# Kernel tuning notes

Measured on AMD Instinct MI355X. Metric: run time of the kernel, lower is better.

Reference implementation:

```python
import jax, jax.numpy as jnp
import numpy as np

N, L = 5, 2097152
WIDTH = 11  # max_pool1d kernel width in the original


def setup_inputs() -> dict:
    key = jax.random.key(0)
    k1, k2 = jax.random.split(key)
    rppg = jax.random.normal(k1, (N, L), dtype=jnp.float32)
    ppg = jax.random.normal(k2, (N, L), dtype=jnp.float32)
    return {"rppg": rppg, "ppg": ppg, "fs": 30, "epoch": 15}


def _normalize(x):
    # normalize_torch: per-signal standardization
    mu = x.mean(axis=1, keepdims=True)
    sd = x.std(axis=1, keepdims=True)
    return (x - mu) / sd


def _window_max(x, width):
    # sliding max over centered window of `width`, same padding (-inf pad)
    return jax.lax.reduce_window(x, -jnp.inf, jax.lax.max,
                                 (1, width), (1, 1),
                                 [(0, 0), (width // 2, width // 2)])


def _mean_hr(x, fs):
    # A position p is a 'nice peak' iff max_pool argmax at p equals p,
    # i.e. x[p] is the max of its own centered window (ties have measure 0
    # for continuous signals). unique()+masking collapses to this mask.
    w = _window_max(x, WIDTH)
    m1 = x == w                                            # [N, L] peak mask
    npk = m1.sum(axis=1, keepdims=True).astype(x.dtype)
    mean_pk = (x * m1).sum(axis=1, keepdims=True) / npk    # mean of peak values
    m = m1 & (x > mean_pk / 2)                             # amplitude-filtered peaks
    idx = jnp.arange(x.shape[1])
    vals = jnp.where(m, idx, -1)
    # previous peak index strictly before p (fixed-shape replacement for diff
    # over a variable-length peak index list)
    prev = jnp.pad(jax.lax.cummax(vals, axis=1)[:, :-1], ((0, 0), (1, 0)),
                   constant_values=-1)
    valid = m & (prev >= 0)                                # one entry per inter-peak gap
    gaps = (idx[None, :] - prev).astype(x.dtype)
    inv = jnp.where(valid, 1.0 / gaps, 0.0)
    # mean(60 / (gap / fs)) = 60 * fs * mean(1 / gap)
    return (60.0 * fs) * inv.sum(axis=1) / valid.sum(axis=1).astype(x.dtype)


def reference(rppg, ppg, fs, epoch):
    ppg = _normalize(ppg.reshape(N, -1))
    rppg = _normalize(rppg.reshape(N, -1))
    ppg_hr = _mean_hr(ppg, fs)
    rppg_hr = _mean_hr(rppg, fs)
    # hr_score = mean_i |ppg_hr - rppg_hr| / ppg_hr  (peak_score is computed
    # in the original but not returned)
    return jnp.mean(jnp.abs(ppg_hr - rppg_hr) / ppg_hr)
```

## Files before the change

### kernel.cpp

```cpp
#include <hip/hip_runtime.h>
#include <math.h>

namespace {

constexpr int LNUM = 2097152;
constexpr int NROW = 5;
constexpr int TPB = 256;
constexpr int CHUNK = 4096;
constexpr int NCHUNK = LNUM / CHUNK;
constexpr int NSERIES = 2 * NROW;
constexpr int NBLK = NSERIES * NCHUNK;
constexpr int NWAVE = TPB / 64;
constexpr int SEG = CHUNK / NWAVE;
constexpr int ITER = SEG / 64;

struct Agg { int first; int last; int c; double s; };

__device__ inline Agg combine(const Agg& a, const Agg& b) {
  Agg r;
  r.first = (a.first >= 0) ? a.first : b.first;
  r.last  = (b.last >= 0) ? b.last : a.last;
  r.s = a.s + b.s;
  r.c = a.c + b.c;
  if (a.last >= 0 && b.first >= 0) {
    r.s += 1.0 / (double)(b.first - a.last);
    r.c += 1;
  }
  return r;
}

__device__ inline void stage(const float* __restrict__ x, int base, float* sh) {
  if (base >= 8 && base + CHUNK + 8 <= LNUM) {
    const float4* xv = (const float4*)(x + base - 8);
    float4* shv = (float4*)sh;
    for (int i = threadIdx.x; i < CHUNK / 4 + 4; i += TPB) shv[i] = xv[i];
  } else {
    for (int i = threadIdx.x; i < CHUNK + 16; i += TPB) {
      int g = base - 8 + i;
      sh[i] = (g >= 0 && g < LNUM) ? x[g] : -INFINITY;
    }
  }
}

__global__ __launch_bounds__(TPB) void stats_kernel(
    const float* __restrict__ rppg, const float* __restrict__ ppg,
    double* __restrict__ psum, double* __restrict__ ppk,
    int* __restrict__ pnpk) {
  __shared__ float sh[CHUNK + 16];
  __shared__ double wsum[NWAVE], wpk[NWAVE];
  __shared__ int wn[NWAVE];
  const int bid = blockIdx.x;
  const int sig = bid / (NROW * NCHUNK);
  const int rem = bid - sig * (NROW * NCHUNK);
  const int row = rem / NCHUNK;
  const int chunk = rem - row * NCHUNK;
  const float* x = (sig == 0 ? rppg : ppg) + (size_t)row * LNUM;
  const int base = chunk * CHUNK;

  stage(x, base, sh);
  __syncthreads();

  const int lane = threadIdx.x & 63;
  const int wid = threadIdx.x >> 6;
  const int woff = wid * SEG;
  double tsum = 0.0, tpk = 0.0;
  int tn = 0;
  for (int j = 0; j < ITER; ++j) {
    int pl = woff + j * 64 + lane;
    float v = sh[pl + 8];
    float w = sh[pl + 3];
#pragma unroll
    for (int k = 1; k < 11; ++k) w = fmaxf(w, sh[pl + 3 + k]);
    tsum += (double)v;
    if (v == w) { tpk += (double)v; ++tn; }
  }
  for (int off = 32; off > 0; off >>= 1) {
    tsum += __shfl_down(tsum, off);
    tpk  += __shfl_down(tpk, off);
    tn   += __shfl_down(tn, off);
  }
  if (lane == 0) { wsum[wid] = tsum; wpk[wid] = tpk; wn[wid] = tn; }
  __syncthreads();
  if (threadIdx.x == 0) {
    double S = 0.0, P = 0.0; int Nn = 0;
    for (int wq = 0; wq < NWAVE; ++wq) { S += wsum[wq]; P += wpk[wq]; Nn += wn[wq]; }
    psum[bid] = S; ppk[bid] = P; pnpk[bid] = Nn;
  }
}

__global__ void thresh_kernel(const double* __restrict__ psum,
                              const double* __restrict__ ppk,
                              const int* __restrict__ pnpk,
                              double* __restrict__ thr) {
  __shared__ double rs[NCHUNK], rp[NCHUNK];
  __shared__ long long rn[NCHUNK];
  const int row = blockIdx.x;
  const int t = threadIdx.x;
  rs[t] = psum[row * NCHUNK + t];
  rp[t] = ppk[row * NCHUNK + t];
  rn[t] = pnpk[row * NCHUNK + t];
  __syncthreads();
  for (int s = NCHUNK / 2; s > 0; s >>= 1) {
    if (t < s) { rs[t] += rs[t + s]; rp[t] += rp[t + s]; rn[t] += rn[t + s]; }
    __syncthreads();
  }
  if (t == 0) {
    double mu = rs[0] / (double)LNUM;
    double mpk = rp[0] / (double)rn[0];
    thr[row] = 0.5 * (mu + mpk);
  }
}

__global__ __launch_bounds__(TPB) void gap_kernel(
    const float* __restrict__ rppg, const float* __restrict__ ppg,
    const double* __restrict__ thr,
    int* __restrict__ cfirst, int* __restrict__ clast,
    double* __restrict__ csum, int* __restrict__ ccnt) {
  __shared__ float sh[CHUNK + 16];
  __shared__ Agg waggs[NWAVE];
  const int bid = blockIdx.x;
  const int sig = bid / (NROW * NCHUNK);
  const int rem = bid - sig * (NROW * NCHUNK);
  const int row = rem / NCHUNK;
  const int chunk = rem - row * NCHUNK;
  const float* x = (sig == 0 ? rppg : ppg) + (size_t)row * LNUM;
  const int base = chunk * CHUNK;
  const float th = (float)thr[sig * NROW + row];

  stage(x, base, sh);
  __syncthreads();

  const int lane = threadIdx.x & 63;
  const int wid = threadIdx.x >> 6;
  const int woff = wid * SEG;
  double lsum = 0.0;
  int lcnt = 0;
  int first = -1, carry = -1;
  for (int j = 0; j < ITER; ++j) {
    int pl = woff + j * 64 + lane;
    float v = sh[pl + 8];
    float w = sh[pl + 3];
#pragma unroll
    for (int k = 1; k < 11; ++k) w = fmaxf(w, sh[pl + 3 + k]);
    bool pk = (v == w) && (v > th);
    unsigned long long bal = __ballot(pk);
    if (pk) {
      unsigned long long below = bal & ((1ull << lane) - 1ull);
      if (below) {
        int prev_lane = 63 - __builtin_clzll(below);
        lsum += 1.0 / (double)(lane - prev_lane);
        ++lcnt;
      } else if (carry >= 0) {
        lsum += 1.0 / (double)(base + pl - carry);
        ++lcnt;
      }
    }
    if (bal) {
      int bb = base + woff + j * 64;
      if (first < 0) first = bb + __builtin_ctzll(bal);
      carry = bb + (63 - __builtin_clzll(bal));
    }
  }
  for (int off = 32; off > 0; off >>= 1) {
    lsum += __shfl_down(lsum, off);
    lcnt += __shfl_down(lcnt, off);
  }
  if (lane == 0) {
    Agg a; a.first = first; a.last = carry; a.c = lcnt; a.s = lsum;
    waggs[wid] = a;
  }
  __syncthreads();
  if (threadIdx.x == 0) {
    Agg a = waggs[0];
    for (int wq = 1; wq < NWAVE; ++wq) a = combine(a, waggs[wq]);
    cfirst[bid] = a.first; clast[bid] = a.last;
    ccnt[bid] = a.c; csum[bid] = a.s;
  }
}

__global__ void finalize_rows(const int* __restrict__ cfirst,
                              const int* __restrict__ clast,
                              const double* __restrict__ csum,
                              const int* __restrict__ ccnt,
                              const int* __restrict__ fsp,
                              double* __restrict__ hr) {
  __shared__ Agg aggs[NCHUNK];
  const int sr = blockIdx.x;
  const int t = threadIdx.x;
  Agg a;
  a.first = cfirst[sr * NCHUNK + t];
  a.last  = clast[sr * NCHUNK + t];
  a.s     = csum[sr * NCHUNK + t];
  a.c     = ccnt[sr * NCHUNK + t];
  aggs[t] = a;
  __syncthreads();
  for (int s = 1; s < NCHUNK; s <<= 1) {
    if ((t & (2 * s - 1)) == 0)
      aggs[t] = combine(aggs[t], aggs[t + s]);
    __syncthreads();
  }
  if (t == 0) {
    double fs = (double)fsp[0];
    hr[sr] = 60.0 * fs * aggs[0].s / (double)aggs[0].c;
  }
}

__global__ void final_kernel(const double* __restrict__ hr,
                             float* __restrict__ out) {
  double acc = 0.0;
  for (int r = 0; r < NROW; ++r) {
    double rh = hr[r];
    double ph = hr[NROW + r];
    acc += fabs(ph - rh) / ph;
  }
  out[0] = (float)(acc / (double)NROW);
}

}

extern "C" void kernel_launch(void* const* d_in, const int* in_sizes, int n_in,
                              void* d_out, int out_size, void* d_ws, size_t ws_size,
                              hipStream_t stream) {
  const float* rppg = (const float*)d_in[0];
  const float* ppg  = (const float*)d_in[1];
  const int* fsp    = (const int*)d_in[2];
  float* out        = (float*)d_out;
  char* ws          = (char*)d_ws;

  double* psum  = (double*)(ws);
  double* ppk   = (double*)(ws + 40960);
  int*    pnpk  = (int*)(ws + 81920);
  double* csum  = (double*)(ws + 102400);
  int*    cfirst= (int*)(ws + 143360);
  int*    clast = (int*)(ws + 163840);
  int*    ccnt  = (int*)(ws + 184320);
  double* thr   = (double*)(ws + 204800);
  double* hr    = (double*)(ws + 205824);

  stats_kernel<<<NBLK, TPB, 0, stream>>>(rppg, ppg, psum, ppk, pnpk);
  thresh_kernel<<<NSERIES, NCHUNK, 0, stream>>>(psum, ppk, pnpk, thr);
  gap_kernel<<<NBLK, TPB, 0, stream>>>(rppg, ppg, thr, cfirst, clast, csum, ccnt);
  finalize_rows<<<NSERIES, NCHUNK, 0, stream>>>(cfirst, clast, csum, ccnt, fsp, hr);
  final_kernel<<<1, 1, 0, stream>>>(hr, out);
  (void)in_sizes; (void)n_in; (void)out_size; (void)ws_size;
}
```

Before: 173.4 us.

## Register-window sliding max with shuffles and fuse reduction kernels via last-block pattern

Replaces shared-memory staging with per-thread float4 loads of 16 contiguous elements. Window halos are exchanged through lane shuffles, and the 11-wide max is built as a log-step max tree in registers. Per-thread gap aggregation becomes sequential within each thread plus a shuffle-based associative combine. The threshold and finalize kernels are folded into the tail of the stats and gap kernels using an atomic counter and last-block reduction, which cuts five launches to two plus a memset. This removes LDS traffic and launch gaps, at the cost of higher register pressure and a serialized last-block tail.

Measured after the change: 384.5 us. +121.8%, slower.

```diff
diff --git a/kernel.cpp b/kernel.cpp
--- a/kernel.cpp
+++ b/kernel.cpp
@@ -5,18 +5,16 @@
 
 constexpr int LNUM = 2097152;
 constexpr int NROW = 5;
+constexpr int NSER = 10;
 constexpr int TPB = 256;
-constexpr int CHUNK = 4096;
-constexpr int NCHUNK = LNUM / CHUNK;
-constexpr int NSERIES = 2 * NROW;
-constexpr int NBLK = NSERIES * NCHUNK;
-constexpr int NWAVE = TPB / 64;
-constexpr int SEG = CHUNK / NWAVE;
-constexpr int ITER = SEG / 64;
+constexpr int EPL = 16;
+constexpr int CHUNK = TPB * EPL;
+constexpr int CPR = LNUM / CHUNK;
+constexpr int NBLK = NSER * CPR;
 
 struct Agg { int first; int last; int c; double s; };
 
-__device__ inline Agg combine(const Agg& a, const Agg& b) {
+__device__ __forceinline__ Agg combine(const Agg& a, const Agg& b) {
   Agg r;
   r.first = (a.first >= 0) ? a.first : b.first;
   r.last  = (b.last >= 0) ? b.last : a.last;
@@ -29,85 +27,119 @@
   return r;
 }
 
-__device__ inline void stage(const float* __restrict__ x, int base, float* sh) {
-  if (base >= 8 && base + CHUNK + 8 <= LNUM) {
-    const float4* xv = (const float4*)(x + base - 8);
-    float4* shv = (float4*)sh;
-    for (int i = threadIdx.x; i < CHUNK / 4 + 4; i += TPB) shv[i] = xv[i];
-  } else {
-    for (int i = threadIdx.x; i < CHUNK + 16; i += TPB) {
-      int g = base - 8 + i;
-      sh[i] = (g >= 0 && g < LNUM) ? x[g] : -INFINITY;
-    }
-  }
+__device__ __forceinline__ void window16(const float* __restrict__ x, int s,
+                                         float X[26], float w[16]) {
+  const float4* q = reinterpret_cast<const float4*>(x + s);
+  float4 f0 = q[0], f1 = q[1], f2 = q[2], f3 = q[3];
+  X[5] = f0.x;  X[6] = f0.y;  X[7] = f0.z;  X[8] = f0.w;
+  X[9] = f1.x;  X[10] = f1.y; X[11] = f1.z; X[12] = f1.w;
+  X[13] = f2.x; X[14] = f2.y; X[15] = f2.z; X[16] = f2.w;
+  X[17] = f3.x; X[18] = f3.y; X[19] = f3.z; X[20] = f3.w;
+#pragma unroll
+  for (int j = 0; j < 5; ++j) X[j] = __shfl_up(X[16 + j], 1);
+#pragma unroll
+  for (int j = 0; j < 5; ++j) X[21 + j] = __shfl_down(X[5 + j], 1);
+  const int lane = threadIdx.x & 63;
+  if (lane == 0) {
+#pragma unroll
+    for (int j = 0; j < 5; ++j) {
+      int g = s - 5 + j;
+      X[j] = (g >= 0) ? x[g] : -INFINITY;
+    }
+  }
+  if (lane == 63) {
+#pragma unroll
+    for (int j = 0; j < 5; ++j) {
+      int g = s + 16 + j;
+      X[21 + j] = (g < LNUM) ? x[g] : -INFINITY;
+    }
+  }
+  float m2[25];
+#pragma unroll
+  for (int i = 0; i < 25; ++i) m2[i] = fmaxf(X[i], X[i + 1]);
+  float m4[23];
+#pragma unroll
+  for (int i = 0; i < 23; ++i) m4[i] = fmaxf(m2[i], m2[i + 2]);
+  float m8[19];
+#pragma unroll
+  for (int i = 0; i < 19; ++i) m8[i] = fmaxf(m4[i], m4[i + 4]);
+#pragma unroll
+  for (int t = 0; t < 16; ++t) w[t] = fmaxf(m8[t], m8[t + 3]);
+}
+
+__device__ __forceinline__ const float* row_ptr(const float* rppg,
+                                                const float* ppg, int rw) {
+  return (rw < NROW) ? rppg + (size_t)rw * LNUM
+                     : ppg + (size_t)(rw - NROW) * LNUM;
 }
 
 __global__ __launch_bounds__(TPB) void stats_kernel(
     const float* __restrict__ rppg, const float* __restrict__ ppg,
     double* __restrict__ psum, double* __restrict__ ppk,
-    int* __restrict__ pnpk) {
-  __shared__ float sh[CHUNK + 16];
-  __shared__ double wsum[NWAVE], wpk[NWAVE];
-  __shared__ int wn[NWAVE];
+    int* __restrict__ pnpk, double* __restrict__ thr,
+    int* __restrict__ counter) {
   const int bid = blockIdx.x;
-  const int sig = bid / (NROW * NCHUNK);
-  const int rem = bid - sig * (NROW * NCHUNK);
-  const int row = rem / NCHUNK;
-  const int chunk = rem - row * NCHUNK;
-  const float* x = (sig == 0 ? rppg : ppg) + (size_t)row * LNUM;
-  const int base = chunk * CHUNK;
-
-  stage(x, base, sh);
-  __syncthreads();
-
+  const int rw = bid >> 9;
+  const int chunk = bid & (CPR - 1);
+  const float* x = row_ptr(rppg, ppg, rw);
   const int lane = threadIdx.x & 63;
   const int wid = threadIdx.x >> 6;
-  const int woff = wid * SEG;
+  const int s = chunk * CHUNK + wid * (64 * EPL) + lane * EPL;
+
+  float X[26], w[16];
+  window16(x, s, X, w);
+
   double tsum = 0.0, tpk = 0.0;
   int tn = 0;
-  for (int j = 0; j < ITER; ++j) {
-    int pl = woff + j * 64 + lane;
-    float v = sh[pl + 8];
-    float w = sh[pl + 3];
-#pragma unroll
-    for (int k = 1; k < 11; ++k) w = fmaxf(w, sh[pl + 3 + k]);
+#pragma unroll
+  for (int t = 0; t < 16; ++t) {
+    float v = X[5 + t];
     tsum += (double)v;
-    if (v == w) { tpk += (double)v; ++tn; }
-  }
+    if (v == w[t]) { tpk += (double)v; ++tn; }
+  }
+#pragma unroll
   for (int off = 32; off > 0; off >>= 1) {
     tsum += __shfl_down(tsum, off);
     tpk  += __shfl_down(tpk, off);
     tn   += __shfl_down(tn, off);
   }
+
+  __shared__ double wsum[4], wpk[4];
+  __shared__ int wn[4];
+  __shared__ int lastFlag;
   if (lane == 0) { wsum[wid] = tsum; wpk[wid] = tpk; wn[wid] = tn; }
   __syncthreads();
   if (threadIdx.x == 0) {
-    double S = 0.0, P = 0.0; int Nn = 0;
-    for (int wq = 0; wq < NWAVE; ++wq) { S += wsum[wq]; P += wpk[wq]; Nn += wn[wq]; }
-    psum[bid] = S; ppk[bid] = P; pnpk[bid] = Nn;
-  }
-}
-
-__global__ void thresh_kernel(const double* __restrict__ psum,
-                              const double* __restrict__ ppk,
-                              const int* __restrict__ pnpk,
-                              double* __restrict__ thr) {
-  __shared__ double rs[NCHUNK], rp[NCHUNK];
-  __shared__ long long rn[NCHUNK];
-  const int row = blockIdx.x;
+    psum[bid] = wsum[0] + wsum[1] + wsum[2] + wsum[3];
+    ppk[bid]  = wpk[0] + wpk[1] + wpk[2] + wpk[3];
+    pnpk[bid] = wn[0] + wn[1] + wn[2] + wn[3];
+    __threadfence();
+    lastFlag = (atomicAdd(counter, 1) == NBLK - 1);
+  }
+  __syncthreads();
+  if (!lastFlag) return;
+  __threadfence();
+
   const int t = threadIdx.x;
-  rs[t] = psum[row * NCHUNK + t];
-  rp[t] = ppk[row * NCHUNK + t];
-  rn[t] = pnpk[row * NCHUNK + t];
-  __syncthreads();
-  for (int s = NCHUNK / 2; s > 0; s >>= 1) {
-    if (t < s) { rs[t] += rs[t + s]; rp[t] += rp[t + s]; rn[t] += rn[t + s]; }
-    __syncthreads();
-  }
-  if (t == 0) {
-    double mu = rs[0] / (double)LNUM;
-    double mpk = rp[0] / (double)rn[0];
-    thr[row] = 0.5 * (mu + mpk);
+  for (int r = 0; r < NSER; ++r) {
+    double s0 = psum[r * CPR + t] + psum[r * CPR + t + 256];
+    double p0 = ppk[r * CPR + t] + ppk[r * CPR + t + 256];
+    int n0 = pnpk[r * CPR + t] + pnpk[r * CPR + t + 256];
+#pragma unroll
+    for (int off = 32; off > 0; off >>= 1) {
+      s0 += __shfl_down(s0, off);
+      p0 += __shfl_down(p0, off);
+      n0 += __shfl_down(n0, off);
+    }
+    if (lane == 0) { wsum[wid] = s0; wpk[wid] = p0; wn[wid] = n0; }
+    __syncthreads();
+    if (t == 0) {
+      double S = wsum[0] + wsum[1] + wsum[2] + wsum[3];
+      double P = wpk[0] + wpk[1] + wpk[2] + wpk[3];
+      double Nn = (double)(wn[0] + wn[1] + wn[2] + wn[3]);
+      thr[r] = 0.5 * (S / (double)LNUM + P / Nn);
+    }
+    __syncthreads();
   }
 }
 
@@ -115,105 +147,95 @@
     const float* __restrict__ rppg, const float* __restrict__ ppg,
     const double* __restrict__ thr,
     int* __restrict__ cfirst, int* __restrict__ clast,
-    double* __restrict__ csum, int* __restrict__ ccnt) {
-  __shared__ float sh[CHUNK + 16];
-  __shared__ Agg waggs[NWAVE];
+    double* __restrict__ csum, int* __restrict__ ccnt,
+    const int* __restrict__ fsp, float* __restrict__ out,
+    int* __restrict__ counter) {
   const int bid = blockIdx.x;
-  const int sig = bid / (NROW * NCHUNK);
-  const int rem = bid - sig * (NROW * NCHUNK);
-  const int row = rem / NCHUNK;
-  const int chunk = rem - row * NCHUNK;
-  const float* x = (sig == 0 ? rppg : ppg) + (size_t)row * LNUM;
-  const int base = chunk * CHUNK;
-  const float th = (float)thr[sig * NROW + row];
-
-  stage(x, base, sh);
-  __syncthreads();
-
+  const int rw = bid >> 9;
+  const int chunk = bid & (CPR - 1);
+  const float* x = row_ptr(rppg, ppg, rw);
+  const float th = (float)thr[rw];
   const int lane = threadIdx.x & 63;
   const int wid = threadIdx.x >> 6;
-  const int woff = wid * SEG;
-  double lsum = 0.0;
-  int lcnt = 0;
-  int first = -1, carry = -1;
-  for (int j = 0; j < ITER; ++j) {
-    int pl = woff + j * 64 + lane;
-    float v = sh[pl + 8];
-    float w = sh[pl + 3];
-#pragma unroll
-    for (int k = 1; k < 11; ++k) w = fmaxf(w, sh[pl + 3 + k]);
-    bool pk = (v == w) && (v > th);
-    unsigned long long bal = __ballot(pk);
-    if (pk) {
-      unsigned long long below = bal & ((1ull << lane) - 1ull);
-      if (below) {
-        int prev_lane = 63 - __builtin_clzll(below);
-        lsum += 1.0 / (double)(lane - prev_lane);
-        ++lcnt;
-      } else if (carry >= 0) {
-        lsum += 1.0 / (double)(base + pl - carry);
-        ++lcnt;
-      }
-    }
-    if (bal) {
-      int bb = base + woff + j * 64;
-      if (first < 0) first = bb + __builtin_ctzll(bal);
-      carry = bb + (63 - __builtin_clzll(bal));
-    }
-  }
-  for (int off = 32; off > 0; off >>= 1) {
-    lsum += __shfl_down(lsum, off);
-    lcnt += __shfl_down(lcnt, off);
-  }
-  if (lane == 0) {
-    Agg a; a.first = first; a.last = carry; a.c = lcnt; a.s = lsum;
-    waggs[wid] = a;
-  }
+  const int s = chunk * CHUNK + wid * (64 * EPL) + lane * EPL;
+
+  float X[26], w[16];
+  window16(x, s, X, w);
+
+  Agg a; a.first = -1; a.last = -1; a.c = 0; a.s = 0.0;
+#pragma unroll
+  for (int t = 0; t < 16; ++t) {
+    float v = X[5 + t];
+    if (v == w[t] && v > th) {
+      int p = s + t;
+      if (a.last >= 0) { a.s += 1.0 / (double)(p - a.last); ++a.c; }
+      else a.first = p;
+      a.last = p;
+    }
+  }
+#pragma unroll
+  for (int off = 1; off < 64; off <<= 1) {
+    Agg b;
+    b.first = __shfl_down(a.first, off);
+    b.last  = __shfl_down(a.last, off);
+    b.c     = __shfl_down(a.c, off);
+    b.s     = __shfl_down(a.s, off);
+    a = combine(a, b);
+  }
+
+  __shared__ Agg waggs[4];
+  __shared__ double shr[NSER];
+  __shared__ int lastFlag;
+  if (lane == 0) waggs[wid] = a;
   __syncthreads();
   if (threadIdx.x == 0) {
-    Agg a = waggs[0];
-    for (int wq = 1; wq < NWAVE; ++wq) a = combine(a, waggs[wq]);
-    cfirst[bid] = a.first; clast[bid] = a.last;
-    ccnt[bid] = a.c; csum[bid] = a.s;
-  }
-}
-
-__global__ void finalize_rows(const int* __restrict__ cfirst,
-                              const int* __restrict__ clast,
-                              const double* __restrict__ csum,
-                              const int* __restrict__ ccnt,
-                              const int* __restrict__ fsp,
-                              double* __restrict__ hr) {
-  __shared__ Agg aggs[NCHUNK];
-  const int sr = blockIdx.x;
+    Agg r = waggs[0];
+    r = combine(r, waggs[1]);
+    r = combine(r, waggs[2]);
+    r = combine(r, waggs[3]);
+    cfirst[bid] = r.first; clast[bid] = r.last;
+    csum[bid] = r.s; ccnt[bid] = r.c;
+    __threadfence();
+    lastFlag = (atomicAdd(counter, 1) == NBLK - 1);
+  }
+  __syncthreads();
+  if (!lastFlag) return;
+  __threadfence();
+
   const int t = threadIdx.x;
-  Agg a;
-  a.first = cfirst[sr * NCHUNK + t];
-  a.last  = clast[sr * NCHUNK + t];
-  a.s     = csum[sr * NCHUNK + t];
-  a.c     = ccnt[sr * NCHUNK + t];
-  aggs[t] = a;
-  __syncthreads();
-  for (int s = 1; s < NCHUNK; s <<= 1) {
-    if ((t & (2 * s - 1)) == 0)
-      aggs[t] = combine(aggs[t], aggs[t + s]);
+  for (int r = 0; r < NSER; ++r) {
+    const int i0 = r * CPR + 2 * t;
+    Agg a0; a0.first = cfirst[i0];     a0.last = clast[i0];
+    a0.c = ccnt[i0];                   a0.s = csum[i0];
+    Agg a1; a1.first = cfirst[i0 + 1]; a1.last = clast[i0 + 1];
+    a1.c = ccnt[i0 + 1];               a1.s = csum[i0 + 1];
+    a0 = combine(a0, a1);
+#pragma unroll
+    for (int off = 1; off < 64; off <<= 1) {
+      Agg b;
+      b.first = __shfl_down(a0.first, off);
+      b.last  = __shfl_down(a0.last, off);
+      b.c     = __shfl_down(a0.c, off);
+      b.s     = __shfl_down(a0.s, off);
+      a0 = combine(a0, b);
+    }
+    if (lane == 0) waggs[wid] = a0;
+    __syncthreads();
+    if (t == 0) {
+      Agg rr = waggs[0];
+      rr = combine(rr, waggs[1]);
+      rr = combine(rr, waggs[2]);
+      rr = combine(rr, waggs[3]);
+      shr[r] = 60.0 * (double)fsp[0] * rr.s / (double)rr.c;
+    }
     __syncthreads();
   }
   if (t == 0) {
-    double fs = (double)fsp[0];
-    hr[sr] = 60.0 * fs * aggs[0].s / (double)aggs[0].c;
-  }
-}
-
-__global__ void final_kernel(const double* __restrict__ hr,
-                             float* __restrict__ out) {
-  double acc = 0.0;
-  for (int r = 0; r < NROW; ++r) {
-    double rh = hr[r];
-    double ph = hr[NROW + r];
-    acc += fabs(ph - rh) / ph;
-  }
-  out[0] = (float)(acc / (double)NROW);
+    double acc = 0.0;
+    for (int r = 0; r < NROW; ++r)
+      acc += fabs(shr[NROW + r] - shr[r]) / shr[NROW + r];
+    out[0] = (float)(acc / (double)NROW);
+  }
 }
 
 }
@@ -227,20 +249,20 @@
   float* out        = (float*)d_out;
   char* ws          = (char*)d_ws;
 
-  double* psum  = (double*)(ws);
-  double* ppk   = (double*)(ws + 40960);
-  int*    pnpk  = (int*)(ws + 81920);
-  double* csum  = (double*)(ws + 102400);
-  int*    cfirst= (int*)(ws + 143360);
-  int*    clast = (int*)(ws + 163840);
-  int*    ccnt  = (int*)(ws + 184320);
-  double* thr   = (double*)(ws + 204800);
-  double* hr    = (double*)(ws + 205824);
-
-  stats_kernel<<<NBLK, TPB, 0, stream>>>(rppg, ppg, psum, ppk, pnpk);
-  thresh_kernel<<<NSERIES, NCHUNK, 0, stream>>>(psum, ppk, pnpk, thr);
-  gap_kernel<<<NBLK, TPB, 0, stream>>>(rppg, ppg, thr, cfirst, clast, csum, ccnt);
-  finalize_rows<<<NSERIES, NCHUNK, 0, stream>>>(cfirst, clast, csum, ccnt, fsp, hr);
-  final_kernel<<<1, 1, 0, stream>>>(hr, out);
+  double* psum   = (double*)(ws);
+  double* ppk    = (double*)(ws + 40960);
+  int*    pnpk   = (int*)(ws + 81920);
+  double* csum   = (double*)(ws + 102400);
+  int*    cfirst = (int*)(ws + 143360);
+  int*    clast  = (int*)(ws + 163840);
+  int*    ccnt   = (int*)(ws + 184320);
+  double* thr    = (double*)(ws + 204800);
+  int*    counters = (int*)(ws + 204928);
+
+  hipMemsetAsync(counters, 0, 2 * sizeof(int), stream);
+  stats_kernel<<<NBLK, TPB, 0, stream>>>(rppg, ppg, psum, ppk, pnpk, thr,
+                                         counters + 0);
+  gap_kernel<<<NBLK, TPB, 0, stream>>>(rppg, ppg, thr, cfirst, clast, csum,
+                                       ccnt, fsp, out, counters + 1);
   (void)in_sizes; (void)n_in; (void)out_size; (void)ws_size;
 }
```
